# Performance work log

Hardware: AMD Instinct MI355X
Metric: run time of the kernel (lower is better)

## Reference

```python
import jax, jax.numpy as jnp
import numpy as np

B, QL, CL = 4, 256, 512
XD, ED, DIM, YD = 128, 128, 128, 16


def setup_inputs() -> dict:
    key = jax.random.key(0)
    ks = jax.random.split(key, 9)
    s = lambda fan_in: 1.0 / np.sqrt(fan_in)
    return {
        "q": jax.random.normal(ks[0], (B, QL, XD), jnp.float32),
        "f_embed": jax.random.normal(ks[1], (B, CL, ED), jnp.float32),
        "att_logits": jax.random.normal(ks[2], (B, QL, CL), jnp.float32),
        # layer 1 of concat-MLP, split into per-branch blocks (same math as concat@W1)
        "W1q": jax.random.normal(ks[3], (XD, DIM), jnp.float32) * s(XD + ED),
        "W1f": jax.random.normal(ks[4], (ED, DIM), jnp.float32) * s(XD + ED),
        "b1": jnp.zeros((DIM,), jnp.float32),
        "W2": jax.random.normal(ks[5], (DIM, DIM), jnp.float32) * s(DIM),
        "b2": jnp.zeros((DIM,), jnp.float32),
        "Wout": jax.random.normal(ks[6], (DIM, 2 * YD), jnp.float32) * s(DIM),
        "bout": jnp.zeros((2 * YD,), jnp.float32),
    }


def reference(q, f_embed, att_logits, W1q, W1f, b1, W2, b2, Wout, bout):
    # First layer: concat([tile(q), tile(f)]) @ W1 == q@W1q (+) f@W1f broadcast-added.
    qp = jnp.einsum("bqd,dh->bqh", q, W1q)            # [B,Q,H]
    fp = jnp.einsum("bcd,dh->bch", f_embed, W1f)      # [B,C,H]
    h = jax.nn.relu(qp[:, :, None, :] + fp[:, None, :, :] + b1)   # [B,Q,C,H]
    h = jax.nn.relu(jnp.einsum("bqch,hk->bqck", h, W2) + b2)      # [B,Q,C,H]
    out = jnp.einsum("bqch,hy->bqcy", h, Wout) + bout             # [B,Q,C,2Y]
    mu, s = jnp.split(out, 2, axis=-1)                            # [B,Q,C,Y] each
    sigma = jax.nn.softplus(jnp.maximum(-15.0, s))
    # MixtureSameFamily(Categorical(att_logits), MVNDiag(mu, sigma)).sample()
    kcat, keps = jax.random.split(jax.random.key(1))
    idx = jax.random.categorical(kcat, att_logits, axis=-1)       # [B,Q]
    gather = lambda t: jnp.take_along_axis(t, idx[:, :, None, None], axis=2)[:, :, 0, :]
    mu_sel, sig_sel = gather(mu), gather(sigma)                   # [B,Q,Y]
    eps = jax.random.normal(keps, mu_sel.shape, mu_sel.dtype)
    y_hat = mu_sel + sig_sel * eps                                # [B,Q,Y]
    return y_hat
```

## Files before the change

### kernel.cpp

```cpp
#include <hip/hip_runtime.h>
#include <stdint.h>

#define Bc   4
#define QLc  256
#define CLc  512
#define Dc   128
#define YDc  16
#define NROW (Bc * QLc)
#define NFP  (Bc * CLc)

__device__ __forceinline__ uint32_t rotl32(uint32_t x, int d) {
  return (x << d) | (x >> (32 - d));
}

__device__ __forceinline__ void tf2x32(uint32_t k0, uint32_t k1, uint32_t x0,
                                       uint32_t x1, uint32_t& o0, uint32_t& o1) {
  const uint32_t k2 = k0 ^ k1 ^ 0x1BD11BDAu;
  uint32_t v0 = x0 + k0, v1 = x1 + k1;
  v0 += v1; v1 = rotl32(v1, 13); v1 ^= v0;
  v0 += v1; v1 = rotl32(v1, 15); v1 ^= v0;
  v0 += v1; v1 = rotl32(v1, 26); v1 ^= v0;
  v0 += v1; v1 = rotl32(v1, 6);  v1 ^= v0;
  v0 += k1; v1 += k2 + 1u;
  v0 += v1; v1 = rotl32(v1, 17); v1 ^= v0;
  v0 += v1; v1 = rotl32(v1, 29); v1 ^= v0;
  v0 += v1; v1 = rotl32(v1, 16); v1 ^= v0;
  v0 += v1; v1 = rotl32(v1, 24); v1 ^= v0;
  v0 += k2; v1 += k0 + 2u;
  v0 += v1; v1 = rotl32(v1, 13); v1 ^= v0;
  v0 += v1; v1 = rotl32(v1, 15); v1 ^= v0;
  v0 += v1; v1 = rotl32(v1, 26); v1 ^= v0;
  v0 += v1; v1 = rotl32(v1, 6);  v1 ^= v0;
  v0 += k0; v1 += k1 + 3u;
  v0 += v1; v1 = rotl32(v1, 17); v1 ^= v0;
  v0 += v1; v1 = rotl32(v1, 29); v1 ^= v0;
  v0 += v1; v1 = rotl32(v1, 16); v1 ^= v0;
  v0 += v1; v1 = rotl32(v1, 24); v1 ^= v0;
  v0 += k1; v1 += k2 + 4u;
  v0 += v1; v1 = rotl32(v1, 13); v1 ^= v0;
  v0 += v1; v1 = rotl32(v1, 15); v1 ^= v0;
  v0 += v1; v1 = rotl32(v1, 26); v1 ^= v0;
  v0 += v1; v1 = rotl32(v1, 6);  v1 ^= v0;
  v0 += k2; v1 += k0 + 5u;
  o0 = v0; o1 = v1;
}

__device__ __forceinline__ void subkeys(uint32_t& ck0, uint32_t& ck1,
                                        uint32_t& ek0, uint32_t& ek1) {
  tf2x32(0u, 1u, 0u, 0u, ck0, ck1);
  tf2x32(0u, 1u, 0u, 1u, ek0, ek1);
}

__device__ __forceinline__ uint32_t rbits(uint32_t k0, uint32_t k1, uint32_t i) {
  uint32_t o0, o1;
  tf2x32(k0, k1, 0u, i, o0, o1);
  return o0 ^ o1;
}

__device__ __forceinline__ float bits_to_unit(uint32_t bits) {
  return __uint_as_float((bits >> 9) | 0x3f800000u) - 1.0f;
}

__device__ __forceinline__ float erfinv_f(float x) {
  float w = -__logf((1.0f - x) * (1.0f + x));
  w = -logf((1.0f - x) * (1.0f + x));
  float p;
  if (w < 5.0f) {
    w -= 2.5f;
    p = 2.81022636e-08f;
    p = fmaf(p, w, 3.43273939e-07f);
    p = fmaf(p, w, -3.5233877e-06f);
    p = fmaf(p, w, -4.39150654e-06f);
    p = fmaf(p, w, 0.00021858087f);
    p = fmaf(p, w, -0.00125372503f);
    p = fmaf(p, w, -0.00417768164f);
    p = fmaf(p, w, 0.246640727f);
    p = fmaf(p, w, 1.50140941f);
  } else {
    w = sqrtf(w) - 3.0f;
    p = -0.000200214257f;
    p = fmaf(p, w, 0.000100950558f);
    p = fmaf(p, w, 0.00134934322f);
    p = fmaf(p, w, -0.00367342844f);
    p = fmaf(p, w, 0.00573950773f);
    p = fmaf(p, w, -0.0076224613f);
    p = fmaf(p, w, 0.00943887047f);
    p = fmaf(p, w, 1.00167406f);
    p = fmaf(p, w, 2.83297682f);
  }
  return p * x;
}

__global__ __launch_bounds__(128) void k_pre(
    const float* __restrict__ q, const float* __restrict__ f,
    const float* __restrict__ logits, const float* __restrict__ W1q,
    const float* __restrict__ W1f, float* __restrict__ ws_fp,
    float* __restrict__ ws_qp, int* __restrict__ ws_idx) {
  const int blk = blockIdx.x;
  const int tid = threadIdx.x;
  __shared__ float sx[8][Dc];
  __shared__ float sv[128];
  __shared__ int   si[128];

  if (blk < 384) {
    const bool is_f = (blk < 256);
    const int row0 = is_f ? blk * 8 : (blk - 256) * 8;
    const float* X = is_f ? f : q;
    const float* W = is_f ? W1f : W1q;
    float* O = is_f ? ws_fp : ws_qp;
#pragma unroll
    for (int r = 0; r < 8; ++r) sx[r][tid] = X[(row0 + r) * Dc + tid];
    __syncthreads();
    float acc[8] = {0.f, 0.f, 0.f, 0.f, 0.f, 0.f, 0.f, 0.f};
    for (int h = 0; h < Dc; ++h) {
      const float w = W[h * Dc + tid];
#pragma unroll
      for (int r = 0; r < 8; ++r) acc[r] = fmaf(sx[r][h], w, acc[r]);
    }
#pragma unroll
    for (int r = 0; r < 8; ++r) O[(row0 + r) * Dc + tid] = acc[r];
  } else {
    const int bq = blk - 384;
    uint32_t ck0, ck1, ek0, ek1;
    subkeys(ck0, ck1, ek0, ek1);
    float best = -3.4e38f;
    int bi = 1 << 30;
#pragma unroll
    for (int j = 0; j < 4; ++j) {
      const int c = tid + j * 128;
      const uint32_t i = (uint32_t)(bq * CLc + c);
      const uint32_t bits = rbits(ck0, ck1, i);
      float fl = bits_to_unit(bits);
      float u = fmaxf(1.17549435e-38f, fl);
      float g = -logf(-logf(u));
      float val = g + logits[i];
      if (val > best || (val == best && c < bi)) { best = val; bi = c; }
    }
    sv[tid] = best; si[tid] = bi;
    __syncthreads();
    for (int s = 64; s > 0; s >>= 1) {
      if (tid < s) {
        const float v2 = sv[tid + s];
        const int i2 = si[tid + s];
        if (v2 > sv[tid] || (v2 == sv[tid] && i2 < si[tid])) {
          sv[tid] = v2; si[tid] = i2;
        }
      }
      __syncthreads();
    }
    if (tid == 0) ws_idx[bq] = si[0];
  }
}

__global__ __launch_bounds__(128) void k_mlp(
    const float* __restrict__ ws_fp, const float* __restrict__ ws_qp,
    const int* __restrict__ ws_idx, const float* __restrict__ b1,
    const float* __restrict__ W2, const float* __restrict__ b2,
    const float* __restrict__ Wout, const float* __restrict__ bout,
    float* __restrict__ out) {
  const int blk = blockIdx.x;
  const int tid = threadIdx.x;
  const int row0 = blk * 8;
  __shared__ float sh[8][Dc];
  __shared__ float so[8][32];
  __shared__ int sidx[8];

  if (tid < 8) sidx[tid] = ws_idx[row0 + tid];
  __syncthreads();

  const float bias1 = b1[tid];
#pragma unroll
  for (int r = 0; r < 8; ++r) {
    const int row = row0 + r;
    const int b = row >> 8;
    const int c = sidx[r];
    const float v = ws_qp[row * Dc + tid] + ws_fp[(b * CLc + c) * Dc + tid] + bias1;
    sh[r][tid] = fmaxf(v, 0.0f);
  }
  __syncthreads();

  float acc[8];
  const float bias2 = b2[tid];
#pragma unroll
  for (int r = 0; r < 8; ++r) acc[r] = bias2;
  for (int h = 0; h < Dc; ++h) {
    const float w = W2[h * Dc + tid];
#pragma unroll
    for (int r = 0; r < 8; ++r) acc[r] = fmaf(sh[r][h], w, acc[r]);
  }
  __syncthreads();
#pragma unroll
  for (int r = 0; r < 8; ++r) sh[r][tid] = fmaxf(acc[r], 0.0f);
  __syncthreads();

  {
    const int k = tid & 31, rg = tid >> 5;
    const int r0 = rg * 2, r1 = rg * 2 + 1;
    float o0 = bout[k], o1 = o0;
    for (int h = 0; h < Dc; ++h) {
      const float w = Wout[h * 32 + k];
      o0 = fmaf(sh[r0][h], w, o0);
      o1 = fmaf(sh[r1][h], w, o1);
    }
    so[r0][k] = o0; so[r1][k] = o1;
  }
  __syncthreads();

  {
    const int r = tid >> 4, y = tid & 15;
    const int row = row0 + r;
    const float mu = so[r][y];
    const float s = so[r][16 + y];
    const float sm = fmaxf(-15.0f, s);
    const float sigma = fmaxf(sm, 0.0f) + log1pf(expf(-fabsf(sm)));

    uint32_t ck0, ck1, ek0, ek1;
    subkeys(ck0, ck1, ek0, ek1);
    const uint32_t i = (uint32_t)(row * YDc + y);
    const uint32_t bits = rbits(ek0, ek1, i);
    const float fl = bits_to_unit(bits);
    const float lo = -0.999999940395355224609375f;
    const float prod = __fmul_rn(fl, 2.0f);
    const float u = fmaxf(lo, __fadd_rn(prod, lo));
    const float eps = 1.4142135623730951f * erfinv_f(u);
    out[row * YDc + y] = mu + sigma * eps;
  }
}

extern "C" void kernel_launch(void* const* d_in, const int* in_sizes, int n_in,
                              void* d_out, int out_size, void* d_ws, size_t ws_size,
                              hipStream_t stream) {
  const float* q      = (const float*)d_in[0];
  const float* f      = (const float*)d_in[1];
  const float* logits = (const float*)d_in[2];
  const float* W1q    = (const float*)d_in[3];
  const float* W1f    = (const float*)d_in[4];
  const float* b1     = (const float*)d_in[5];
  const float* W2     = (const float*)d_in[6];
  const float* b2     = (const float*)d_in[7];
  const float* Wout   = (const float*)d_in[8];
  const float* bout   = (const float*)d_in[9];
  float* out = (float*)d_out;

  float* ws_fp  = (float*)d_ws;
  float* ws_qp  = ws_fp + NFP * Dc;
  int*   ws_idx = (int*)(ws_qp + NROW * Dc);

  k_pre<<<dim3(256 + 128 + NROW), dim3(128), 0, stream>>>(
      q, f, logits, W1q, W1f, ws_fp, ws_qp, ws_idx);
  k_mlp<<<dim3(NROW / 8), dim3(128), 0, stream>>>(
      ws_fp, ws_qp, ws_idx, b1, W2, b2, Wout, bout, out);
}
```

Measured before the change: 97.88 us.

## Fuse sampling and MLP into one kernel, projecting only the selected f row

Merges the pre-pass and MLP kernels into a single kernel where each 256-thread block handles two query rows. It does the categorical argmax first, then computes the f projection only for the selected context row instead of projecting all 2048 f rows. This removes a kernel launch, the workspace round trip and most of the f@W1f work. The trade-off is that weight matrices are re-read per pair of rows with less register reuse, 512 blocks each doing serial dependent phases.

After: 84.59 us. -13.6%, faster.

```diff
diff --git a/kernel.cpp b/kernel.cpp
--- a/kernel.cpp
+++ b/kernel.cpp
@@ -7,7 +7,6 @@
 #define Dc   128
 #define YDc  16
 #define NROW (Bc * QLc)
-#define NFP  (Bc * CLc)
 
 __device__ __forceinline__ uint32_t rotl32(uint32_t x, int d) {
   return (x << d) | (x >> (32 - d));
@@ -62,8 +61,7 @@
 }
 
 __device__ __forceinline__ float erfinv_f(float x) {
-  float w = -__logf((1.0f - x) * (1.0f + x));
-  w = -logf((1.0f - x) * (1.0f + x));
+  float w = -logf((1.0f - x) * (1.0f + x));
   float p;
   if (w < 5.0f) {
     w -= 2.5f;
@@ -91,139 +89,118 @@
   return p * x;
 }
 
-__global__ __launch_bounds__(128) void k_pre(
+__global__ __launch_bounds__(256) void k_fused(
     const float* __restrict__ q, const float* __restrict__ f,
     const float* __restrict__ logits, const float* __restrict__ W1q,
-    const float* __restrict__ W1f, float* __restrict__ ws_fp,
-    float* __restrict__ ws_qp, int* __restrict__ ws_idx) {
-  const int blk = blockIdx.x;
-  const int tid = threadIdx.x;
-  __shared__ float sx[8][Dc];
-  __shared__ float sv[128];
-  __shared__ int   si[128];
-
-  if (blk < 384) {
-    const bool is_f = (blk < 256);
-    const int row0 = is_f ? blk * 8 : (blk - 256) * 8;
-    const float* X = is_f ? f : q;
-    const float* W = is_f ? W1f : W1q;
-    float* O = is_f ? ws_fp : ws_qp;
-#pragma unroll
-    for (int r = 0; r < 8; ++r) sx[r][tid] = X[(row0 + r) * Dc + tid];
-    __syncthreads();
-    float acc[8] = {0.f, 0.f, 0.f, 0.f, 0.f, 0.f, 0.f, 0.f};
-    for (int h = 0; h < Dc; ++h) {
-      const float w = W[h * Dc + tid];
-#pragma unroll
-      for (int r = 0; r < 8; ++r) acc[r] = fmaf(sx[r][h], w, acc[r]);
-    }
-#pragma unroll
-    for (int r = 0; r < 8; ++r) O[(row0 + r) * Dc + tid] = acc[r];
-  } else {
-    const int bq = blk - 384;
-    uint32_t ck0, ck1, ek0, ek1;
-    subkeys(ck0, ck1, ek0, ek1);
-    float best = -3.4e38f;
-    int bi = 1 << 30;
-#pragma unroll
-    for (int j = 0; j < 4; ++j) {
-      const int c = tid + j * 128;
-      const uint32_t i = (uint32_t)(bq * CLc + c);
-      const uint32_t bits = rbits(ck0, ck1, i);
-      float fl = bits_to_unit(bits);
-      float u = fmaxf(1.17549435e-38f, fl);
-      float g = -logf(-logf(u));
-      float val = g + logits[i];
-      if (val > best || (val == best && c < bi)) { best = val; bi = c; }
-    }
-    sv[tid] = best; si[tid] = bi;
-    __syncthreads();
-    for (int s = 64; s > 0; s >>= 1) {
-      if (tid < s) {
-        const float v2 = sv[tid + s];
-        const int i2 = si[tid + s];
-        if (v2 > sv[tid] || (v2 == sv[tid] && i2 < si[tid])) {
-          sv[tid] = v2; si[tid] = i2;
-        }
-      }
-      __syncthreads();
-    }
-    if (tid == 0) ws_idx[bq] = si[0];
-  }
-}
-
-__global__ __launch_bounds__(128) void k_mlp(
-    const float* __restrict__ ws_fp, const float* __restrict__ ws_qp,
-    const int* __restrict__ ws_idx, const float* __restrict__ b1,
+    const float* __restrict__ W1f, const float* __restrict__ b1,
     const float* __restrict__ W2, const float* __restrict__ b2,
     const float* __restrict__ Wout, const float* __restrict__ bout,
     float* __restrict__ out) {
-  const int blk = blockIdx.x;
   const int tid = threadIdx.x;
-  const int row0 = blk * 8;
-  __shared__ float sh[8][Dc];
-  __shared__ float so[8][32];
-  __shared__ int sidx[8];
-
-  if (tid < 8) sidx[tid] = ws_idx[row0 + tid];
-  __syncthreads();
-
-  const float bias1 = b1[tid];
+  const int r   = tid >> 7;
+  const int l   = tid & 127;
+  const int row = blockIdx.x * 2 + r;
+  const int b   = row >> 8;
+
+  __shared__ float sx[2][Dc];
+  __shared__ float sh[2][Dc];
+  __shared__ float sv[256];
+  __shared__ int   si[256];
+  __shared__ float spart[2][4][32];
+  __shared__ float so[2][32];
+  __shared__ int   sc[2];
+
+  const float qv = q[row * Dc + l];
+
+  uint32_t ck0, ck1, ek0, ek1;
+  subkeys(ck0, ck1, ek0, ek1);
+
+  float best = -3.4e38f;
+  int bi = 1 << 30;
 #pragma unroll
-  for (int r = 0; r < 8; ++r) {
-    const int row = row0 + r;
-    const int b = row >> 8;
-    const int c = sidx[r];
-    const float v = ws_qp[row * Dc + tid] + ws_fp[(b * CLc + c) * Dc + tid] + bias1;
-    sh[r][tid] = fmaxf(v, 0.0f);
-  }
-  __syncthreads();
-
-  float acc[8];
-  const float bias2 = b2[tid];
+  for (int j = 0; j < 4; ++j) {
+    const int c = l + j * 128;
+    const uint32_t i = (uint32_t)(row * CLc + c);
+    const uint32_t bits = rbits(ck0, ck1, i);
+    const float fl = bits_to_unit(bits);
+    const float u = fmaxf(1.17549435e-38f, fl);
+    const float g = -logf(-logf(u));
+    const float val = g + logits[i];
+    if (val > best || (val == best && c < bi)) { best = val; bi = c; }
+  }
+  sv[tid] = best; si[tid] = bi;
+  __syncthreads();
+  for (int s = 64; s > 0; s >>= 1) {
+    if (l < s) {
+      const int a0 = r * 128 + l, a1 = a0 + s;
+      const float v2 = sv[a1];
+      const int i2 = si[a1];
+      if (v2 > sv[a0] || (v2 == sv[a0] && i2 < si[a0])) {
+        sv[a0] = v2; si[a0] = i2;
+      }
+    }
+    __syncthreads();
+  }
+  if (l == 0) sc[r] = si[r * 128];
+
+  sx[r][l] = qv;
+  __syncthreads();
+  float acc1 = 0.0f;
+  for (int h = 0; h < Dc; ++h) acc1 = fmaf(sx[r][h], W1q[h * Dc + l], acc1);
+
+  const int csel = sc[r];
+  const float fv = f[(b * CLc + csel) * Dc + l];
+  __syncthreads();
+  sx[r][l] = fv;
+  __syncthreads();
+  float accf = 0.0f;
+  for (int h = 0; h < Dc; ++h) accf = fmaf(sx[r][h], W1f[h * Dc + l], accf);
+
+  sh[r][l] = fmaxf(acc1 + accf + b1[l], 0.0f);
+  __syncthreads();
+
+  float acc2 = b2[l];
+  for (int h = 0; h < Dc; ++h) acc2 = fmaf(sh[r][h], W2[h * Dc + l], acc2);
+  __syncthreads();
+  sh[r][l] = fmaxf(acc2, 0.0f);
+  __syncthreads();
+
+  {
+    const int k  = tid & 31;
+    const int rr = (tid >> 5) & 1;
+    const int g  = tid >> 6;
+    float p = 0.0f;
 #pragma unroll
-  for (int r = 0; r < 8; ++r) acc[r] = bias2;
-  for (int h = 0; h < Dc; ++h) {
-    const float w = W2[h * Dc + tid];
-#pragma unroll
-    for (int r = 0; r < 8; ++r) acc[r] = fmaf(sh[r][h], w, acc[r]);
-  }
-  __syncthreads();
-#pragma unroll
-  for (int r = 0; r < 8; ++r) sh[r][tid] = fmaxf(acc[r], 0.0f);
-  __syncthreads();
-
-  {
-    const int k = tid & 31, rg = tid >> 5;
-    const int r0 = rg * 2, r1 = rg * 2 + 1;
-    float o0 = bout[k], o1 = o0;
-    for (int h = 0; h < Dc; ++h) {
-      const float w = Wout[h * 32 + k];
-      o0 = fmaf(sh[r0][h], w, o0);
-      o1 = fmaf(sh[r1][h], w, o1);
+    for (int hh = 0; hh < 32; ++hh) {
+      const int h = g * 32 + hh;
+      p = fmaf(sh[rr][h], Wout[h * 32 + k], p);
     }
-    so[r0][k] = o0; so[r1][k] = o1;
-  }
-  __syncthreads();
-
-  {
-    const int r = tid >> 4, y = tid & 15;
-    const int row = row0 + r;
-    const float mu = so[r][y];
-    const float s = so[r][16 + y];
+    spart[rr][g][k] = p;
+  }
+  __syncthreads();
+  if (tid < 64) {
+    const int rr = tid >> 5, k = tid & 31;
+    so[rr][k] = bout[k] + spart[rr][0][k] + spart[rr][1][k] +
+                spart[rr][2][k] + spart[rr][3][k];
+  }
+  __syncthreads();
+
+  if (tid < 32) {
+    const int rr = tid >> 4, y = tid & 15;
+    const int orow = blockIdx.x * 2 + rr;
+    const float mu = so[rr][y];
+    const float s  = so[rr][16 + y];
     const float sm = fmaxf(-15.0f, s);
     const float sigma = fmaxf(sm, 0.0f) + log1pf(expf(-fabsf(sm)));
 
-    uint32_t ck0, ck1, ek0, ek1;
-    subkeys(ck0, ck1, ek0, ek1);
-    const uint32_t i = (uint32_t)(row * YDc + y);
+    const uint32_t i = (uint32_t)(orow * YDc + y);
     const uint32_t bits = rbits(ek0, ek1, i);
     const float fl = bits_to_unit(bits);
     const float lo = -0.999999940395355224609375f;
     const float prod = __fmul_rn(fl, 2.0f);
     const float u = fmaxf(lo, __fadd_rn(prod, lo));
     const float eps = 1.4142135623730951f * erfinv_f(u);
-    out[row * YDc + y] = mu + sigma * eps;
+    out[orow * YDc + y] = mu + sigma * eps;
   }
 }
 
@@ -242,12 +219,6 @@
   const float* bout   = (const float*)d_in[9];
   float* out = (float*)d_out;
 
-  float* ws_fp  = (float*)d_ws;
-  float* ws_qp  = ws_fp + NFP * Dc;
-  int*   ws_idx = (int*)(ws_qp + NROW * Dc);
-
-  k_pre<<<dim3(256 + 128 + NROW), dim3(128), 0, stream>>>(
-      q, f, logits, W1q, W1f, ws_fp, ws_qp, ws_idx);
-  k_mlp<<<dim3(NROW / 8), dim3(128), 0, stream>>>(
-      ws_fp, ws_qp, ws_idx, b1, W2, b2, Wout, bout, out);
-}
+  k_fused<<<dim3(NROW / 2), dim3(256), 0, stream>>>(
+      q, f, logits, W1q, W1f, b1, W2, b2, Wout, bout, out);
+}
```
